# Performance work log

Hardware: AMD Instinct MI355X
Metric: run time of the kernel (lower is better)

Reference implementation:

```python
import jax, jax.numpy as jnp
import numpy as np

EP = 1e-4
MAX_ITER = 100
L = [512, 512]          # context lengths
C = 256                 # padded feature dim == total_dim
HEADS = 2


def nonsat_activation(x, ep=EP, max_iter=MAX_ITER):
    # Fixed-point iteration y <- (2y^3/3 + x)/(y^2+1), y0 = x.
    # Matches torch version: iterate on detached values, final update uses live x.
    xd = jax.lax.stop_gradient(x)
    f = lambda y: (2.0 * y ** 3 / 3.0 + xd) / (y ** 2 + 1.0)

    def cond(s):
        y, y_new, i = s
        return jnp.logical_and(jnp.mean(jnp.abs(y_new - y)) > ep, i <= max_iter)

    def body(s):
        y, y_new, i = s
        return (y_new, f(y_new), i + 1)

    y_prev, _, _ = jax.lax.while_loop(cond, body, (xd, f(xd), 0))
    y_prev = jax.lax.stop_gradient(y_prev)
    # final (returned) update, differentiable w.r.t. x only
    return (2.0 * y_prev ** 3 / 3.0 + x) / (y_prev ** 2 + 1.0)


def setup_inputs() -> dict:
    key = jax.random.key(0)
    k1, k2, k3 = jax.random.split(key, 3)
    x1 = jax.random.normal(k1, (32, 512, 256), dtype=jnp.float32)
    x2 = jax.random.normal(k2, (32, 512, 192), dtype=jnp.float32)
    # xavier_normal_ for U: std = sqrt(2/(fan_in+fan_out)) = sqrt(2/512) = 1/16
    U = jax.random.normal(k3, (HEADS, C, C), dtype=jnp.float32) * (1.0 / 16.0)
    return {"x1": x1, "x2": x2, "U": U}


def reference(x1, x2, U):
    # pad contexts to common feature dim C (zeros on the right)
    contexts = [x1, jnp.pad(x2, ((0, 0), (0, 0), (0, C - x2.shape[-1])))]
    q = sum(L)
    scaling = C ** (-0.5)
    M = jnp.concatenate(contexts, axis=1)  # (B, q, C)

    # mask uses sizes = L[1:] with blocks starting at offset 0 (faithful quirk)
    mask_mul = jnp.ones((q, q), dtype=jnp.float32).at[:L[1], :L[1]].set(0.0)

    h_reps = []
    mask_add = None
    for h in range(HEADS):
        # K[b,i,j] = sum_{c,d} M[b,i,c] U[h,c,d] M[b,j,d]
        K = jnp.einsum('bic,cd,bjd->bij', M, U[h], M) * scaling
        K = nonsat_activation(K)
        if mask_add is None:  # cached after head 0, reused for later heads
            mask_add = jnp.zeros((q, q), dtype=jnp.float32).at[:L[1], :L[1]].set(jnp.min(K))
        K_hat = K * mask_mul + mask_add
        cols = jnp.max(K_hat, axis=1)   # (B, q) max over rows per column
        rows = jnp.max(K_hat, axis=2)   # (B, q) max over cols per row
        alpha = rows + cols             # (B, q)
        reps = []
        offset = 0
        for i, Ci in enumerate(contexts):
            a = alpha[:, offset:offset + L[i]]          # (B, l_i)
            offset += L[i]
            wt = jax.nn.softmax(a, axis=1)              # (B, l_i)
            r = jnp.einsum('bl,blc->bc', wt, Ci)        # (B, C)
            reps.append(r)
        h_reps.append(jnp.stack(reps, axis=1))          # (B, N, C)
    return jnp.stack(h_reps, axis=0)                    # (heads, B, N, C)
```

## Files before the change

kernel.cpp:

```cpp
#include <hip/hip_runtime.h>
#include <math.h>

typedef _Float16 h16;
typedef h16  h16x8 __attribute__((ext_vector_type(8)));
typedef h16  h16x4 __attribute__((ext_vector_type(4)));
typedef float f32x4 __attribute__((ext_vector_type(4)));

#define MH_OFF   ((size_t)0)
#define ML_OFF   (MH_OFF + 16777216)
#define UHT_OFF  (ML_OFF + 16777216)
#define ULT_OFF  (UHT_OFF + 262144)
#define RMA_OFF  (ULT_OFF + 262144)
#define RMH_OFF  (RMA_OFF + 262144)
#define PCM_OFF  (RMH_OFF + 262144)
#define M0_OFF   (PCM_OFF + 4194304)

__device__ __forceinline__ float nonsat(float x) {
    float y = x;
#pragma unroll
    for (int i = 0; i < 24; ++i) {
        float y2 = y * y;
        y = fmaf(0.66666667f * y, y2, x) / (y2 + 1.0f);
    }
    return y;
}

__device__ __forceinline__ int fkey(float f) {
    const int i = __float_as_int(f);
    return (i >= 0) ? i : (i ^ 0x7fffffff);
}
__device__ __forceinline__ float funkey(int k) {
    return __int_as_float((k >= 0) ? k : (k ^ 0x7fffffff));
}

__global__ void k_prep(const float* __restrict__ x1, const float* __restrict__ x2,
                       const float* __restrict__ U, h16* __restrict__ MH,
                       h16* __restrict__ ML, h16* __restrict__ UHt,
                       h16* __restrict__ ULt, int* __restrict__ m0key,
                       float* __restrict__ out) {
    const int gid = blockIdx.x * 256 + threadIdx.x;
    if (blockIdx.x < 8192) {
        const int g  = gid;
        const int d4 = (g & 63) * 4;
        const int j  = (g >> 6) & 1023;
        const int b  = g >> 16;
        float v[4];
        if (j < 512) {
            const float4 p = *(const float4*)(x1 + ((size_t)(b * 512 + j) * 256 + d4));
            v[0] = p.x; v[1] = p.y; v[2] = p.z; v[3] = p.w;
        } else if (d4 < 192) {
            const float4 p = *(const float4*)(x2 +
                (size_t)(b * 512 + (j - 512)) * 192 + d4);
            v[0] = p.x; v[1] = p.y; v[2] = p.z; v[3] = p.w;
        } else {
            v[0] = v[1] = v[2] = v[3] = 0.0f;
        }
        h16x4 hh, ll;
#pragma unroll
        for (int k = 0; k < 4; ++k) {
            const h16 hi = (h16)v[k];
            hh[k] = hi;
            ll[k] = (h16)(v[k] - (float)hi);
        }
        const size_t o = (size_t)g * 4;
        *(h16x4*)&MH[o] = hh;
        *(h16x4*)&ML[o] = ll;
    } else if (blockIdx.x < 8320) {
        const int g  = gid - 8192 * 256;
        const int c4 = (g & 63) * 4;
        const int d  = (g >> 6) & 255;
        const int h  = g >> 14;
        h16x4 hh, ll;
#pragma unroll
        for (int k = 0; k < 4; ++k) {
            const float v = U[((size_t)h * 256 + c4 + k) * 256 + d] * 4.0f;
            const h16 hi = (h16)v;
            hh[k] = hi;
            ll[k] = (h16)(v - (float)hi);
        }
        const size_t o = ((size_t)h * 256 + d) * 256 + c4;
        *(h16x4*)&UHt[o] = hh;
        *(h16x4*)&ULt[o] = ll;
    } else {
        const int z = gid - 8320 * 256;
        out[z] = 0.0f;
        if (z == 0) *m0key = 0x7fffffff;
    }
}

__global__ __launch_bounds__(256, 2)
void k_main(const h16* __restrict__ MH, const h16* __restrict__ ML,
            const h16* __restrict__ UHt, const h16* __restrict__ ULt,
            float* __restrict__ rmax_all, float* __restrict__ rmax_hi,
            float* __restrict__ pcm, int* __restrict__ m0key) {
    __shared__ __align__(16) h16 sP[2][64 * 256];
    __shared__ float red[512 + 4];

    const int n    = blockIdx.x;
    const int x    = n & 7;
    const int s    = n >> 3;
    const int b    = x + 8 * (s >> 5);
    const int h    = (s >> 4) & 1;
    const int rblk = s & 15;
    const int hb   = h * 32 + b;
    const int r0   = rblk * 64;
    const int t    = threadIdx.x;
    const int w    = t >> 6;
    const int l    = t & 63;
    const int q    = l >> 4;
    const int ln   = l & 15;

    {
        f32x4 acc[4][4];
        const f32x4 z4 = {0.f, 0.f, 0.f, 0.f};
#pragma unroll
        for (int i = 0; i < 4; ++i)
#pragma unroll
            for (int j = 0; j < 4; ++j) acc[i][j] = z4;

        for (int kc = 0; kc < 8; ++kc) {
            const int c0 = kc * 32;
            h16x8 aH[4], aL[4], bH[4], bL[4];
#pragma unroll
            for (int ti = 0; ti < 4; ++ti) {
                const size_t off =
                    (size_t)(b * 1024 + r0 + ti * 16 + ln) * 256 + c0 + q * 8;
                aH[ti] = *(const h16x8*)&MH[off];
                aL[ti] = *(const h16x8*)&ML[off];
            }
#pragma unroll
            for (int tj = 0; tj < 4; ++tj) {
                const size_t off =
                    (size_t)(h * 256 + w * 64 + tj * 16 + ln) * 256 + c0 + q * 8;
                bH[tj] = *(const h16x8*)&UHt[off];
                bL[tj] = *(const h16x8*)&ULt[off];
            }
#pragma unroll
            for (int ti = 0; ti < 4; ++ti)
#pragma unroll
                for (int tj = 0; tj < 4; ++tj)
                    acc[ti][tj] = __builtin_amdgcn_mfma_f32_16x16x32_f16(
                        aH[ti], bH[tj], acc[ti][tj], 0, 0, 0);
#pragma unroll
            for (int ti = 0; ti < 4; ++ti)
#pragma unroll
                for (int tj = 0; tj < 4; ++tj)
                    acc[ti][tj] = __builtin_amdgcn_mfma_f32_16x16x32_f16(
                        aL[ti], bH[tj], acc[ti][tj], 0, 0, 0);
#pragma unroll
            for (int ti = 0; ti < 4; ++ti)
#pragma unroll
                for (int tj = 0; tj < 4; ++tj)
                    acc[ti][tj] = __builtin_amdgcn_mfma_f32_16x16x32_f16(
                        aH[ti], bL[tj], acc[ti][tj], 0, 0, 0);
        }
#pragma unroll
        for (int ti = 0; ti < 4; ++ti)
#pragma unroll
            for (int tj = 0; tj < 4; ++tj)
#pragma unroll
                for (int reg = 0; reg < 4; ++reg) {
                    const int r = ti * 16 + q * 4 + reg;
                    const int d = w * 64 + tj * 16 + ln;
                    const float v = acc[ti][tj][reg];
                    const h16 hi = (h16)v;
                    const h16 lo = (h16)(v - (float)hi);
                    const int off = r * 256 + (((d >> 3) ^ (r & 7)) << 3) + (d & 7);
                    sP[0][off] = hi;
                    sP[1][off] = lo;
                }
    }
    __syncthreads();

    float gmin = INFINITY;
    const int jts = (h == 1 && rblk < 8) ? 1 : 0;

    for (int jt = jts; jt < 2; ++jt) {
        const int jbase = jt * 512 + w * 128;
        const bool do_red = (rblk >= 8) || (jt == 1);
        f32x4 acc[4][8];
        const f32x4 z4 = {0.f, 0.f, 0.f, 0.f};
#pragma unroll
        for (int i = 0; i < 4; ++i)
#pragma unroll
            for (int j = 0; j < 8; ++j) acc[i][j] = z4;

        for (int kc = 0; kc < 8; ++kc) {
            const int d0 = kc * 32;
            h16x8 aH[4], aL[4], bb[8];
#pragma unroll
            for (int ti = 0; ti < 4; ++ti) {
                const int r = ti * 16 + ln;
                const int g = (kc * 4 + q) ^ (r & 7);
                aH[ti] = *(const h16x8*)&sP[0][r * 256 + g * 8];
                aL[ti] = *(const h16x8*)&sP[1][r * 256 + g * 8];
            }
#pragma unroll
            for (int tj = 0; tj < 8; ++tj)
                bb[tj] = *(const h16x8*)&MH[
                    (size_t)(b * 1024 + jbase + tj * 16 + ln) * 256 + d0 + q * 8];
#pragma unroll
            for (int tj = 0; tj < 8; ++tj)
#pragma unroll
                for (int ti = 0; ti < 4; ++ti)
                    acc[ti][tj] = __builtin_amdgcn_mfma_f32_16x16x32_f16(
                        aH[ti], bb[tj], acc[ti][tj], 0, 0, 0);
#pragma unroll
            for (int tj = 0; tj < 8; ++tj)
#pragma unroll
                for (int ti = 0; ti < 4; ++ti)
                    acc[ti][tj] = __builtin_amdgcn_mfma_f32_16x16x32_f16(
                        aL[ti], bb[tj], acc[ti][tj], 0, 0, 0);
#pragma unroll
            for (int tj = 0; tj < 8; ++tj)
                bb[tj] = *(const h16x8*)&ML[
                    (size_t)(b * 1024 + jbase + tj * 16 + ln) * 256 + d0 + q * 8];
#pragma unroll
            for (int tj = 0; tj < 8; ++tj)
#pragma unroll
                for (int ti = 0; ti < 4; ++ti)
                    acc[ti][tj] = __builtin_amdgcn_mfma_f32_16x16x32_f16(
                        aH[ti], bb[tj], acc[ti][tj], 0, 0, 0);
        }

        if (do_red) {
#pragma unroll
            for (int ti = 0; ti < 4; ++ti)
#pragma unroll
                for (int reg = 0; reg < 4; ++reg) {
                    float m = acc[ti][0][reg];
#pragma unroll
                    for (int tj = 1; tj < 8; ++tj) m = fmaxf(m, acc[ti][tj][reg]);
                    m = fmaxf(m, __shfl_xor(m, 1));
                    m = fmaxf(m, __shfl_xor(m, 2));
                    m = fmaxf(m, __shfl_xor(m, 4));
                    m = fmaxf(m, __shfl_xor(m, 8));
                    if (ln == 0)
                        red[(jt * 4 + w) * 64 + ti * 16 + q * 4 + reg] = m;
                }
#pragma unroll
            for (int tj = 0; tj < 8; ++tj) {
                float m = -INFINITY;
#pragma unroll
                for (int ti = 0; ti < 4; ++ti)
#pragma unroll
                    for (int reg = 0; reg < 4; ++reg) m = fmaxf(m, acc[ti][tj][reg]);
                m = fmaxf(m, __shfl_xor(m, 16));
                m = fmaxf(m, __shfl_xor(m, 32));
                if (q == 0)
                    pcm[(size_t)(hb * 16 + rblk) * 1024 + jbase + tj * 16 + ln] =
                        m * 0.015625f;
            }
        }
        if (h == 0) {
#pragma unroll
            for (int ti = 0; ti < 4; ++ti)
#pragma unroll
                for (int tj = 0; tj < 8; ++tj)
#pragma unroll
                    for (int reg = 0; reg < 4; ++reg)
                        gmin = fminf(gmin, acc[ti][tj][reg]);
        }
    }

#pragma unroll
    for (int off = 1; off < 64; off <<= 1) gmin = fminf(gmin, __shfl_xor(gmin, off));
    if (l == 0) red[512 + w] = gmin;
    __syncthreads();

    if (t < 64) {
        float hh = -INFINITY;
#pragma unroll
        for (int w2 = 0; w2 < 4; ++w2)
            hh = fmaxf(hh, red[(4 + w2) * 64 + t]);
        if (rblk < 8) {
            rmax_hi[(size_t)hb * 1024 + r0 + t] = hh * 0.015625f;
        } else {
            float a = hh;
#pragma unroll
            for (int w2 = 0; w2 < 4; ++w2)
                a = fmaxf(a, red[w2 * 64 + t]);
            rmax_all[(size_t)hb * 1024 + r0 + t] = a * 0.015625f;
        }
    }
    if (t == 0 && hb < 32) {
        const float g4 = fminf(fminf(red[512], red[513]),
                               fminf(red[514], red[515])) * 0.015625f;
        atomicMin(m0key, fkey(g4));
    }
}

__global__ __launch_bounds__(256)
void k_fin(const float* __restrict__ rmax_all, const float* __restrict__ rmax_hi,
           const float* __restrict__ pcm, const int* __restrict__ m0key,
           const float* __restrict__ x1, const float* __restrict__ x2,
           float* __restrict__ out) {
    __shared__ float wv[512];
    __shared__ float sm[4], ss[4];
    const int blk   = blockIdx.x;
    const int chunk = blk & 1;
    const int seg   = (blk >> 1) & 1;
    const int hb    = blk >> 2;
    const int b     = hb & 31;
    const int t     = threadIdx.x;
    const float m0  = funkey(*m0key);

    float a2[2];
#pragma unroll
    for (int half = 0; half < 2; ++half) {
        const int i = seg * 512 + half * 256 + t;
        float rraw;
        if (seg == 0) rraw = fmaxf(m0, rmax_hi[(size_t)hb * 1024 + i]);
        else          rraw = rmax_all[(size_t)hb * 1024 + i];
        float call = -INFINITY, chi = -INFINITY;
#pragma unroll
        for (int rb = 0; rb < 16; ++rb) {
            const float v = pcm[(size_t)(hb * 16 + rb) * 1024 + i];
            call = fmaxf(call, v);
            if (rb >= 8) chi = fmaxf(chi, v);
        }
        const float craw = (seg == 0) ? fmaxf(m0, chi) : call;
        a2[half] = nonsat(rraw) + nonsat(craw);
    }
    const float a0 = a2[0], a1 = a2[1];

    float m = fmaxf(a0, a1);
#pragma unroll
    for (int off = 1; off < 64; off <<= 1) m = fmaxf(m, __shfl_xor(m, off));
    if ((t & 63) == 0) sm[t >> 6] = m;
    __syncthreads();
    const float amax = fmaxf(fmaxf(sm[0], sm[1]), fmaxf(sm[2], sm[3]));

    const float e0 = __expf(a0 - amax), e1 = __expf(a1 - amax);
    wv[t] = e0; wv[t + 256] = e1;
    float s = e0 + e1;
#pragma unroll
    for (int off = 1; off < 64; off <<= 1) s += __shfl_xor(s, off);
    if ((t & 63) == 0) ss[t >> 6] = s;
    __syncthreads();
    const float inv = 1.0f / (ss[0] + ss[1] + ss[2] + ss[3]);

    const int lo = chunk * 256;
    float acc = 0.0f;
    if (seg == 0) {
        const float* xp = x1 + ((size_t)b * 512 + lo) * 256 + t;
#pragma unroll 4
        for (int l = 0; l < 256; ++l)
            acc = fmaf(wv[lo + l], xp[(size_t)l * 256], acc);
        atomicAdd(&out[(hb * 2 + seg) * 256 + t], acc * inv);
    } else if (t < 192) {
        const float* xp = x2 + ((size_t)b * 512 + lo) * 192 + t;
#pragma unroll 4
        for (int l = 0; l < 256; ++l)
            acc = fmaf(wv[lo + l], xp[(size_t)l * 192], acc);
        atomicAdd(&out[(hb * 2 + seg) * 256 + t], acc * inv);
    }
}

extern "C" void kernel_launch(void* const* d_in, const int* in_sizes, int n_in,
                              void* d_out, int out_size, void* d_ws, size_t ws_size,
                              hipStream_t stream) {
    const float* x1 = (const float*)d_in[0];
    const float* x2 = (const float*)d_in[1];
    const float* U  = (const float*)d_in[2];
    float* out = (float*)d_out;
    char* wsb  = (char*)d_ws;

    h16*   MHp  = (h16*)(wsb + MH_OFF);
    h16*   MLp  = (h16*)(wsb + ML_OFF);
    h16*   UHt  = (h16*)(wsb + UHT_OFF);
    h16*   ULt  = (h16*)(wsb + ULT_OFF);
    float* rma  = (float*)(wsb + RMA_OFF);
    float* rmh  = (float*)(wsb + RMH_OFF);
    float* pcm  = (float*)(wsb + PCM_OFF);
    int*   m0k  = (int*)(wsb + M0_OFF);

    hipLaunchKernelGGL(k_prep, dim3(8448), dim3(256), 0, stream, x1, x2, U,
                       MHp, MLp, UHt, ULt, m0k, out);
    hipLaunchKernelGGL(k_main, dim3(1024), dim3(256), 0, stream, MHp, MLp,
                       UHt, ULt, rma, rmh, pcm, m0k);
    hipLaunchKernelGGL(k_fin,  dim3(256),  dim3(256), 0, stream, rma, rmh,
                       pcm, m0k, x1, x2, out);
}
```

Before: 280.8 us.

## Split k_main work across 16 waves per block instead of 4

Raises the k_main block size from 256 to 1024 threads and redistributes both GEMM phases so each wave owns a smaller tile: the first phase splits 4 row tiles by 4 column groups, and the second gives each wave 32 columns instead of 128. Reduction buffers and final cross-wave reductions grow to cover 16 waves. The aim is to cut per-wave register pressure and give more latency hiding per CU. The cost is that each wave reloads the LDS A-fragments and now reuses them over only 2 B tiles, so operand reuse per MFMA drops. It also raises LDS read traffic and the barrier cost within a block.

```diff
diff --git a/kernel.cpp b/kernel.cpp
--- a/kernel.cpp
+++ b/kernel.cpp
@@ -88,13 +88,13 @@
     }
 }
 
-__global__ __launch_bounds__(256, 2)
+__global__ __launch_bounds__(1024, 4)
 void k_main(const h16* __restrict__ MH, const h16* __restrict__ ML,
             const h16* __restrict__ UHt, const h16* __restrict__ ULt,
             float* __restrict__ rmax_all, float* __restrict__ rmax_hi,
             float* __restrict__ pcm, int* __restrict__ m0key) {
     __shared__ __align__(16) h16 sP[2][64 * 256];
-    __shared__ float red[512 + 4];
+    __shared__ float red[2048 + 16];
 
     const int n    = blockIdx.x;
     const int x    = n & 7;
@@ -111,64 +111,54 @@
     const int ln   = l & 15;
 
     {
-        f32x4 acc[4][4];
+        const int wr = w >> 2, wc = w & 3;
+        f32x4 acc[4];
         const f32x4 z4 = {0.f, 0.f, 0.f, 0.f};
 #pragma unroll
-        for (int i = 0; i < 4; ++i)
-#pragma unroll
-            for (int j = 0; j < 4; ++j) acc[i][j] = z4;
+        for (int j = 0; j < 4; ++j) acc[j] = z4;
 
         for (int kc = 0; kc < 8; ++kc) {
             const int c0 = kc * 32;
-            h16x8 aH[4], aL[4], bH[4], bL[4];
-#pragma unroll
-            for (int ti = 0; ti < 4; ++ti) {
+            h16x8 aH, aL, bH[4], bL[4];
+            {
                 const size_t off =
-                    (size_t)(b * 1024 + r0 + ti * 16 + ln) * 256 + c0 + q * 8;
-                aH[ti] = *(const h16x8*)&MH[off];
-                aL[ti] = *(const h16x8*)&ML[off];
+                    (size_t)(b * 1024 + r0 + wr * 16 + ln) * 256 + c0 + q * 8;
+                aH = *(const h16x8*)&MH[off];
+                aL = *(const h16x8*)&ML[off];
             }
 #pragma unroll
             for (int tj = 0; tj < 4; ++tj) {
                 const size_t off =
-                    (size_t)(h * 256 + w * 64 + tj * 16 + ln) * 256 + c0 + q * 8;
+                    (size_t)(h * 256 + wc * 64 + tj * 16 + ln) * 256 + c0 + q * 8;
                 bH[tj] = *(const h16x8*)&UHt[off];
                 bL[tj] = *(const h16x8*)&ULt[off];
             }
 #pragma unroll
-            for (int ti = 0; ti < 4; ++ti)
-#pragma unroll
-                for (int tj = 0; tj < 4; ++tj)
-                    acc[ti][tj] = __builtin_amdgcn_mfma_f32_16x16x32_f16(
-                        aH[ti], bH[tj], acc[ti][tj], 0, 0, 0);
-#pragma unroll
-            for (int ti = 0; ti < 4; ++ti)
-#pragma unroll
-                for (int tj = 0; tj < 4; ++tj)
-                    acc[ti][tj] = __builtin_amdgcn_mfma_f32_16x16x32_f16(
-                        aL[ti], bH[tj], acc[ti][tj], 0, 0, 0);
-#pragma unroll
-            for (int ti = 0; ti < 4; ++ti)
-#pragma unroll
-                for (int tj = 0; tj < 4; ++tj)
-                    acc[ti][tj] = __builtin_amdgcn_mfma_f32_16x16x32_f16(
-                        aH[ti], bL[tj], acc[ti][tj], 0, 0, 0);
-        }
-#pragma unroll
-        for (int ti = 0; ti < 4; ++ti)
-#pragma unroll
             for (int tj = 0; tj < 4; ++tj)
-#pragma unroll
-                for (int reg = 0; reg < 4; ++reg) {
-                    const int r = ti * 16 + q * 4 + reg;
-                    const int d = w * 64 + tj * 16 + ln;
-                    const float v = acc[ti][tj][reg];
-                    const h16 hi = (h16)v;
-                    const h16 lo = (h16)(v - (float)hi);
-                    const int off = r * 256 + (((d >> 3) ^ (r & 7)) << 3) + (d & 7);
-                    sP[0][off] = hi;
-                    sP[1][off] = lo;
-                }
+                acc[tj] = __builtin_amdgcn_mfma_f32_16x16x32_f16(
+                    aH, bH[tj], acc[tj], 0, 0, 0);
+#pragma unroll
+            for (int tj = 0; tj < 4; ++tj)
+                acc[tj] = __builtin_amdgcn_mfma_f32_16x16x32_f16(
+                    aL, bH[tj], acc[tj], 0, 0, 0);
+#pragma unroll
+            for (int tj = 0; tj < 4; ++tj)
+                acc[tj] = __builtin_amdgcn_mfma_f32_16x16x32_f16(
+                    aH, bL[tj], acc[tj], 0, 0, 0);
+        }
+#pragma unroll
+        for (int tj = 0; tj < 4; ++tj)
+#pragma unroll
+            for (int reg = 0; reg < 4; ++reg) {
+                const int r = wr * 16 + q * 4 + reg;
+                const int d = wc * 64 + tj * 16 + ln;
+                const float v = acc[tj][reg];
+                const h16 hi = (h16)v;
+                const h16 lo = (h16)(v - (float)hi);
+                const int off = r * 256 + (((d >> 3) ^ (r & 7)) << 3) + (d & 7);
+                sP[0][off] = hi;
+                sP[1][off] = lo;
+            }
     }
     __syncthreads();
 
@@ -176,47 +166,47 @@
     const int jts = (h == 1 && rblk < 8) ? 1 : 0;
 
     for (int jt = jts; jt < 2; ++jt) {
-        const int jbase = jt * 512 + w * 128;
+        const int jbase = jt * 512 + w * 32;
         const bool do_red = (rblk >= 8) || (jt == 1);
-        f32x4 acc[4][8];
+        f32x4 acc[4][2];
         const f32x4 z4 = {0.f, 0.f, 0.f, 0.f};
 #pragma unroll
         for (int i = 0; i < 4; ++i)
 #pragma unroll
-            for (int j = 0; j < 8; ++j) acc[i][j] = z4;
+            for (int j = 0; j < 2; ++j) acc[i][j] = z4;
 
         for (int kc = 0; kc < 8; ++kc) {
             const int d0 = kc * 32;
-            h16x8 aH[4], aL[4], bb[8];
+            h16x8 aH[4], aL[4], bb[2];
+            const int g = ((kc * 4 + q) ^ (ln & 7)) * 8;
 #pragma unroll
             for (int ti = 0; ti < 4; ++ti) {
                 const int r = ti * 16 + ln;
-                const int g = (kc * 4 + q) ^ (r & 7);
-                aH[ti] = *(const h16x8*)&sP[0][r * 256 + g * 8];
-                aL[ti] = *(const h16x8*)&sP[1][r * 256 + g * 8];
-            }
-#pragma unroll
-            for (int tj = 0; tj < 8; ++tj)
+                aH[ti] = *(const h16x8*)&sP[0][r * 256 + g];
+                aL[ti] = *(const h16x8*)&sP[1][r * 256 + g];
+            }
+#pragma unroll
+            for (int tj = 0; tj < 2; ++tj)
                 bb[tj] = *(const h16x8*)&MH[
                     (size_t)(b * 1024 + jbase + tj * 16 + ln) * 256 + d0 + q * 8];
 #pragma unroll
-            for (int tj = 0; tj < 8; ++tj)
+            for (int tj = 0; tj < 2; ++tj)
 #pragma unroll
                 for (int ti = 0; ti < 4; ++ti)
                     acc[ti][tj] = __builtin_amdgcn_mfma_f32_16x16x32_f16(
                         aH[ti], bb[tj], acc[ti][tj], 0, 0, 0);
 #pragma unroll
-            for (int tj = 0; tj < 8; ++tj)
+            for (int tj = 0; tj < 2; ++tj)
 #pragma unroll
                 for (int ti = 0; ti < 4; ++ti)
                     acc[ti][tj] = __builtin_amdgcn_mfma_f32_16x16x32_f16(
                         aL[ti], bb[tj], acc[ti][tj], 0, 0, 0);
 #pragma unroll
-            for (int tj = 0; tj < 8; ++tj)
+            for (int tj = 0; tj < 2; ++tj)
                 bb[tj] = *(const h16x8*)&ML[
                     (size_t)(b * 1024 + jbase + tj * 16 + ln) * 256 + d0 + q * 8];
 #pragma unroll
-            for (int tj = 0; tj < 8; ++tj)
+            for (int tj = 0; tj < 2; ++tj)
 #pragma unroll
                 for (int ti = 0; ti < 4; ++ti)
                     acc[ti][tj] = __builtin_amdgcn_mfma_f32_16x16x32_f16(
@@ -228,18 +218,16 @@
             for (int ti = 0; ti < 4; ++ti)
 #pragma unroll
                 for (int reg = 0; reg < 4; ++reg) {
-                    float m = acc[ti][0][reg];
-#pragma unroll
-                    for (int tj = 1; tj < 8; ++tj) m = fmaxf(m, acc[ti][tj][reg]);
+                    float m = fmaxf(acc[ti][0][reg], acc[ti][1][reg]);
                     m = fmaxf(m, __shfl_xor(m, 1));
                     m = fmaxf(m, __shfl_xor(m, 2));
                     m = fmaxf(m, __shfl_xor(m, 4));
                     m = fmaxf(m, __shfl_xor(m, 8));
                     if (ln == 0)
-                        red[(jt * 4 + w) * 64 + ti * 16 + q * 4 + reg] = m;
+                        red[(jt * 16 + w) * 64 + ti * 16 + q * 4 + reg] = m;
                 }
 #pragma unroll
-            for (int tj = 0; tj < 8; ++tj) {
+            for (int tj = 0; tj < 2; ++tj) {
                 float m = -INFINITY;
 #pragma unroll
                 for (int ti = 0; ti < 4; ++ti)
@@ -256,7 +244,7 @@
 #pragma unroll
             for (int ti = 0; ti < 4; ++ti)
 #pragma unroll
-                for (int tj = 0; tj < 8; ++tj)
+                for (int tj = 0; tj < 2; ++tj)
 #pragma unroll
                     for (int reg = 0; reg < 4; ++reg)
                         gmin = fminf(gmin, acc[ti][tj][reg]);
@@ -265,28 +253,29 @@
 
 #pragma unroll
     for (int off = 1; off < 64; off <<= 1) gmin = fminf(gmin, __shfl_xor(gmin, off));
-    if (l == 0) red[512 + w] = gmin;
+    if (l == 0) red[2048 + w] = gmin;
     __syncthreads();
 
     if (t < 64) {
         float hh = -INFINITY;
 #pragma unroll
-        for (int w2 = 0; w2 < 4; ++w2)
-            hh = fmaxf(hh, red[(4 + w2) * 64 + t]);
+        for (int w2 = 0; w2 < 16; ++w2)
+            hh = fmaxf(hh, red[(16 + w2) * 64 + t]);
         if (rblk < 8) {
             rmax_hi[(size_t)hb * 1024 + r0 + t] = hh * 0.015625f;
         } else {
             float a = hh;
 #pragma unroll
-            for (int w2 = 0; w2 < 4; ++w2)
+            for (int w2 = 0; w2 < 16; ++w2)
                 a = fmaxf(a, red[w2 * 64 + t]);
             rmax_all[(size_t)hb * 1024 + r0 + t] = a * 0.015625f;
         }
     }
     if (t == 0 && hb < 32) {
-        const float g4 = fminf(fminf(red[512], red[513]),
-                               fminf(red[514], red[515])) * 0.015625f;
-        atomicMin(m0key, fkey(g4));
+        float g4 = red[2048];
+#pragma unroll
+        for (int i = 1; i < 16; ++i) g4 = fminf(g4, red[2048 + i]);
+        atomicMin(m0key, fkey(g4 * 0.015625f));
     }
 }
 
@@ -377,7 +366,7 @@
 
     hipLaunchKernelGGL(k_prep, dim3(8448), dim3(256), 0, stream, x1, x2, U,
                        MHp, MLp, UHt, ULt, m0k, out);
-    hipLaunchKernelGGL(k_main, dim3(1024), dim3(256), 0, stream, MHp, MLp,
+    hipLaunchKernelGGL(k_main, dim3(1024), dim3(1024), 0, stream, MHp, MLp,
                        UHt, ULt, rma, rmh, pcm, m0k);
     hipLaunchKernelGGL(k_fin,  dim3(256),  dim3(256), 0, stream, rma, rmh,
                        pcm, m0k, x1, x2, out);
```

Result: slower. 836.6 us (+198.0%).

## Double-buffer M tiles in LDS via async global_load_lds with 512-thread blocks

Applied to the files above, without the earlier changes.

The second GEMM stage no longer reads M hi/lo fragments straight from global memory per wave. Each k-step's 256x32 hi/lo tile is now staged into a double-buffered LDS area with global_load_lds, issued one step ahead. Blocks grow to 512 threads split as a 2x4 wave grid, so each wave holds a smaller accumulator tile. Row and column max reductions are restructured around this, with column maxima merged through shared memory. In exchange there is a barrier every k-step, much larger LDS use that may cap residency at one block per CU, possible bank conflicts on the 64-byte-stride tile reads, and reliance on barrier-implied waits for the async LDS loads.

```diff
diff --git a/kernel.cpp b/kernel.cpp
--- a/kernel.cpp
+++ b/kernel.cpp
@@ -88,13 +88,35 @@
     }
 }
 
-__global__ __launch_bounds__(256, 2)
+__device__ __forceinline__ void stage_b(const h16* __restrict__ MH,
+                                        const h16* __restrict__ ML,
+                                        h16* sBf, int buf, int b, int jt,
+                                        int jtile, int kc, int t, int w) {
+    const int jrow0 = jt * 512 + jtile * 256;
+#pragma unroll
+    for (int g = 0; g < 2; ++g) {
+        const size_t src = (size_t)(b * 1024 + jrow0 + g * 128 + (t >> 2)) * 256
+                           + kc * 32 + (t & 3) * 8;
+        h16* dH = sBf + (size_t)(buf * 2 + 0) * 8192 + g * 4096 + w * 512;
+        h16* dL = sBf + (size_t)(buf * 2 + 1) * 8192 + g * 4096 + w * 512;
+        __builtin_amdgcn_global_load_lds(
+            (const __attribute__((address_space(1))) void*)(MH + src),
+            (__attribute__((address_space(3))) void*)dH, 16, 0, 0);
+        __builtin_amdgcn_global_load_lds(
+            (const __attribute__((address_space(1))) void*)(ML + src),
+            (__attribute__((address_space(3))) void*)dL, 16, 0, 0);
+    }
+}
+
+__global__ __launch_bounds__(512, 2)
 void k_main(const h16* __restrict__ MH, const h16* __restrict__ ML,
             const h16* __restrict__ UHt, const h16* __restrict__ ULt,
             float* __restrict__ rmax_all, float* __restrict__ rmax_hi,
             float* __restrict__ pcm, int* __restrict__ m0key) {
     __shared__ __align__(16) h16 sP[2][64 * 256];
-    __shared__ float red[512 + 4];
+    __shared__ __align__(16) h16 sB[2 * 2 * 8192];
+    __shared__ float red[1024 + 8];
+    __shared__ float scm[2][512];
 
     const int n    = blockIdx.x;
     const int x    = n & 7;
@@ -109,60 +131,68 @@
     const int l    = t & 63;
     const int q    = l >> 4;
     const int ln   = l & 15;
+    const int wr   = w >> 2;
+    const int wj   = w & 3;
+
+    const int jts    = (h == 1 && rblk < 8) ? 1 : 0;
+    const int Usteps = (2 - jts) * 16;
+
+    stage_b(MH, ML, sB, 0, b, jts, 0, 0, t, w);
 
     {
-        f32x4 acc[4][4];
+        const int wrA = w >> 2, wcA = w & 3;
+        f32x4 accA[2][4];
         const f32x4 z4 = {0.f, 0.f, 0.f, 0.f};
 #pragma unroll
-        for (int i = 0; i < 4; ++i)
-#pragma unroll
-            for (int j = 0; j < 4; ++j) acc[i][j] = z4;
+        for (int i = 0; i < 2; ++i)
+#pragma unroll
+            for (int j2 = 0; j2 < 4; ++j2) accA[i][j2] = z4;
 
         for (int kc = 0; kc < 8; ++kc) {
             const int c0 = kc * 32;
-            h16x8 aH[4], aL[4], bH[4], bL[4];
-#pragma unroll
-            for (int ti = 0; ti < 4; ++ti) {
+            h16x8 aH[2], aL[2], bH[4], bL[4];
+#pragma unroll
+            for (int ti = 0; ti < 2; ++ti) {
                 const size_t off =
-                    (size_t)(b * 1024 + r0 + ti * 16 + ln) * 256 + c0 + q * 8;
+                    (size_t)(b * 1024 + r0 + wrA * 32 + ti * 16 + ln) * 256 + c0 + q * 8;
                 aH[ti] = *(const h16x8*)&MH[off];
                 aL[ti] = *(const h16x8*)&ML[off];
             }
 #pragma unroll
             for (int tj = 0; tj < 4; ++tj) {
                 const size_t off =
-                    (size_t)(h * 256 + w * 64 + tj * 16 + ln) * 256 + c0 + q * 8;
+                    (size_t)(h * 256 + wcA * 64 + tj * 16 + ln) * 256 + c0 + q * 8;
                 bH[tj] = *(const h16x8*)&UHt[off];
                 bL[tj] = *(const h16x8*)&ULt[off];
             }
 #pragma unroll
-            for (int ti = 0; ti < 4; ++ti)
+            for (int ti = 0; ti < 2; ++ti)
 #pragma unroll
                 for (int tj = 0; tj < 4; ++tj)
-                    acc[ti][tj] = __builtin_amdgcn_mfma_f32_16x16x32_f16(
-                        aH[ti], bH[tj], acc[ti][tj], 0, 0, 0);
-#pragma unroll
-            for (int ti = 0; ti < 4; ++ti)
+                    accA[ti][tj] = __builtin_amdgcn_mfma_f32_16x16x32_f16(
+                        aH[ti], bH[tj], accA[ti][tj], 0, 0, 0);
+#pragma unroll
+            for (int ti = 0; ti < 2; ++ti)
 #pragma unroll
                 for (int tj = 0; tj < 4; ++tj)
-                    acc[ti][tj] = __builtin_amdgcn_mfma_f32_16x16x32_f16(
-                        aL[ti], bH[tj], acc[ti][tj], 0, 0, 0);
-#pragma unroll
-            for (int ti = 0; ti < 4; ++ti)
+                    accA[ti][tj] = __builtin_amdgcn_mfma_f32_16x16x32_f16(
+                        aL[ti], bH[tj], accA[ti][tj], 0, 0, 0);
+#pragma unroll
+            for (int ti = 0; ti < 2; ++ti)
 #pragma unroll
                 for (int tj = 0; tj < 4; ++tj)
-                    acc[ti][tj] = __builtin_amdgcn_mfma_f32_16x16x32_f16(
-                        aH[ti], bL[tj], acc[ti][tj], 0, 0, 0);
-        }
-#pragma unroll
-        for (int ti = 0; ti < 4; ++ti)
+                    accA[ti][tj] = __builtin_amdgcn_mfma_f32_16x16x32_f16(
+                        aH[ti], bL[tj], accA[ti][tj], 0, 0, 0);
+        }
+#pragma unroll
+        for (int ti = 0; ti < 2; ++ti)
 #pragma unroll
             for (int tj = 0; tj < 4; ++tj)
 #pragma unroll
                 for (int reg = 0; reg < 4; ++reg) {
-                    const int r = ti * 16 + q * 4 + reg;
-                    const int d = w * 64 + tj * 16 + ln;
-                    const float v = acc[ti][tj][reg];
+                    const int r = wrA * 32 + ti * 16 + q * 4 + reg;
+                    const int d = wcA * 64 + tj * 16 + ln;
+                    const float v = accA[ti][tj][reg];
                     const h16 hi = (h16)v;
                     const h16 lo = (h16)(v - (float)hi);
                     const int off = r * 256 + (((d >> 3) ^ (r & 7)) << 3) + (d & 7);
@@ -173,120 +203,151 @@
     __syncthreads();
 
     float gmin = INFINITY;
-    const int jts = (h == 1 && rblk < 8) ? 1 : 0;
-
-    for (int jt = jts; jt < 2; ++jt) {
-        const int jbase = jt * 512 + w * 128;
-        const bool do_red = (rblk >= 8) || (jt == 1);
-        f32x4 acc[4][8];
-        const f32x4 z4 = {0.f, 0.f, 0.f, 0.f};
-#pragma unroll
-        for (int i = 0; i < 4; ++i)
-#pragma unroll
-            for (int j = 0; j < 8; ++j) acc[i][j] = z4;
-
-        for (int kc = 0; kc < 8; ++kc) {
-            const int d0 = kc * 32;
-            h16x8 aH[4], aL[4], bb[8];
-#pragma unroll
-            for (int ti = 0; ti < 4; ++ti) {
-                const int r = ti * 16 + ln;
-                const int g = (kc * 4 + q) ^ (r & 7);
-                aH[ti] = *(const h16x8*)&sP[0][r * 256 + g * 8];
-                aL[ti] = *(const h16x8*)&sP[1][r * 256 + g * 8];
+    float rm[2][4];
+    f32x4 acc[2][4];
+    const f32x4 z4 = {0.f, 0.f, 0.f, 0.f};
+    int cur = 0;
+
+#pragma unroll 1
+    for (int u = 0; u < Usteps; ++u) {
+        const int jt    = jts + (u >> 4);
+        const int jtile = (u >> 3) & 1;
+        const int kc    = u & 7;
+        const bool dored = (rblk >= 8) || (jt == 1);
+
+        if (u + 1 < Usteps) {
+            const int u1 = u + 1;
+            stage_b(MH, ML, sB, cur ^ 1, b, jts + (u1 >> 4), (u1 >> 3) & 1,
+                    u1 & 7, t, w);
+        }
+        if (kc == 0) {
+#pragma unroll
+            for (int i = 0; i < 2; ++i)
+#pragma unroll
+                for (int j2 = 0; j2 < 4; ++j2) acc[i][j2] = z4;
+            if (jtile == 0) {
+#pragma unroll
+                for (int i = 0; i < 2; ++i)
+#pragma unroll
+                    for (int j2 = 0; j2 < 4; ++j2) rm[i][j2] = -INFINITY;
             }
-#pragma unroll
-            for (int tj = 0; tj < 8; ++tj)
-                bb[tj] = *(const h16x8*)&MH[
-                    (size_t)(b * 1024 + jbase + tj * 16 + ln) * 256 + d0 + q * 8];
-#pragma unroll
-            for (int tj = 0; tj < 8; ++tj)
-#pragma unroll
-                for (int ti = 0; ti < 4; ++ti)
-                    acc[ti][tj] = __builtin_amdgcn_mfma_f32_16x16x32_f16(
-                        aH[ti], bb[tj], acc[ti][tj], 0, 0, 0);
-#pragma unroll
-            for (int tj = 0; tj < 8; ++tj)
-#pragma unroll
-                for (int ti = 0; ti < 4; ++ti)
-                    acc[ti][tj] = __builtin_amdgcn_mfma_f32_16x16x32_f16(
-                        aL[ti], bb[tj], acc[ti][tj], 0, 0, 0);
-#pragma unroll
-            for (int tj = 0; tj < 8; ++tj)
-                bb[tj] = *(const h16x8*)&ML[
-                    (size_t)(b * 1024 + jbase + tj * 16 + ln) * 256 + d0 + q * 8];
-#pragma unroll
-            for (int tj = 0; tj < 8; ++tj)
-#pragma unroll
-                for (int ti = 0; ti < 4; ++ti)
-                    acc[ti][tj] = __builtin_amdgcn_mfma_f32_16x16x32_f16(
-                        aH[ti], bb[tj], acc[ti][tj], 0, 0, 0);
-        }
-
-        if (do_red) {
-#pragma unroll
-            for (int ti = 0; ti < 4; ++ti)
-#pragma unroll
-                for (int reg = 0; reg < 4; ++reg) {
-                    float m = acc[ti][0][reg];
-#pragma unroll
-                    for (int tj = 1; tj < 8; ++tj) m = fmaxf(m, acc[ti][tj][reg]);
-                    m = fmaxf(m, __shfl_xor(m, 1));
-                    m = fmaxf(m, __shfl_xor(m, 2));
-                    m = fmaxf(m, __shfl_xor(m, 4));
-                    m = fmaxf(m, __shfl_xor(m, 8));
-                    if (ln == 0)
-                        red[(jt * 4 + w) * 64 + ti * 16 + q * 4 + reg] = m;
+        }
+
+        h16x8 aH[2], aL[2], bH[4], bL[4];
+#pragma unroll
+        for (int ti = 0; ti < 2; ++ti) {
+            const int r = wr * 32 + ti * 16 + ln;
+            const int g = ((kc * 4 + q) ^ (r & 7)) * 8;
+            aH[ti] = *(const h16x8*)&sP[0][r * 256 + g];
+            aL[ti] = *(const h16x8*)&sP[1][r * 256 + g];
+        }
+#pragma unroll
+        for (int tj = 0; tj < 4; ++tj) {
+            const int jr = wj * 64 + tj * 16 + ln;
+            bH[tj] = *(const h16x8*)&sB[(size_t)(cur * 2 + 0) * 8192 + jr * 32 + q * 8];
+            bL[tj] = *(const h16x8*)&sB[(size_t)(cur * 2 + 1) * 8192 + jr * 32 + q * 8];
+        }
+#pragma unroll
+        for (int tj = 0; tj < 4; ++tj)
+#pragma unroll
+            for (int ti = 0; ti < 2; ++ti)
+                acc[ti][tj] = __builtin_amdgcn_mfma_f32_16x16x32_f16(
+                    aH[ti], bH[tj], acc[ti][tj], 0, 0, 0);
+#pragma unroll
+        for (int tj = 0; tj < 4; ++tj)
+#pragma unroll
+            for (int ti = 0; ti < 2; ++ti)
+                acc[ti][tj] = __builtin_amdgcn_mfma_f32_16x16x32_f16(
+                    aL[ti], bH[tj], acc[ti][tj], 0, 0, 0);
+#pragma unroll
+        for (int tj = 0; tj < 4; ++tj)
+#pragma unroll
+            for (int ti = 0; ti < 2; ++ti)
+                acc[ti][tj] = __builtin_amdgcn_mfma_f32_16x16x32_f16(
+                    aH[ti], bL[tj], acc[ti][tj], 0, 0, 0);
+
+        if (kc == 7) {
+            if (dored) {
+#pragma unroll
+                for (int ti = 0; ti < 2; ++ti)
+#pragma unroll
+                    for (int reg = 0; reg < 4; ++reg) {
+                        float m = acc[ti][0][reg];
+#pragma unroll
+                        for (int tj = 1; tj < 4; ++tj) m = fmaxf(m, acc[ti][tj][reg]);
+                        m = fmaxf(m, __shfl_xor(m, 1));
+                        m = fmaxf(m, __shfl_xor(m, 2));
+                        m = fmaxf(m, __shfl_xor(m, 4));
+                        m = fmaxf(m, __shfl_xor(m, 8));
+                        rm[ti][reg] = fmaxf(rm[ti][reg], m);
+                    }
+                if (jtile == 1) {
+#pragma unroll
+                    for (int ti = 0; ti < 2; ++ti)
+#pragma unroll
+                        for (int reg = 0; reg < 4; ++reg)
+                            if (ln == 0)
+                                red[(jt * 8 + w) * 64 + wr * 32 + ti * 16 +
+                                    q * 4 + reg] = rm[ti][reg];
                 }
 #pragma unroll
-            for (int tj = 0; tj < 8; ++tj) {
-                float m = -INFINITY;
-#pragma unroll
-                for (int ti = 0; ti < 4; ++ti)
-#pragma unroll
-                    for (int reg = 0; reg < 4; ++reg) m = fmaxf(m, acc[ti][tj][reg]);
-                m = fmaxf(m, __shfl_xor(m, 16));
-                m = fmaxf(m, __shfl_xor(m, 32));
-                if (q == 0)
-                    pcm[(size_t)(hb * 16 + rblk) * 1024 + jbase + tj * 16 + ln] =
-                        m * 0.015625f;
+                for (int tj = 0; tj < 4; ++tj) {
+                    float m = -INFINITY;
+#pragma unroll
+                    for (int ti = 0; ti < 2; ++ti)
+#pragma unroll
+                        for (int reg = 0; reg < 4; ++reg)
+                            m = fmaxf(m, acc[ti][tj][reg]);
+                    m = fmaxf(m, __shfl_xor(m, 16));
+                    m = fmaxf(m, __shfl_xor(m, 32));
+                    if (q == 0)
+                        scm[wr][jtile * 256 + wj * 64 + tj * 16 + ln] = m;
+                }
             }
-        }
-        if (h == 0) {
-#pragma unroll
-            for (int ti = 0; ti < 4; ++ti)
-#pragma unroll
-                for (int tj = 0; tj < 8; ++tj)
-#pragma unroll
-                    for (int reg = 0; reg < 4; ++reg)
-                        gmin = fminf(gmin, acc[ti][tj][reg]);
+            if (h == 0) {
+#pragma unroll
+                for (int ti = 0; ti < 2; ++ti)
+#pragma unroll
+                    for (int tj = 0; tj < 4; ++tj)
+#pragma unroll
+                        for (int reg = 0; reg < 4; ++reg)
+                            gmin = fminf(gmin, acc[ti][tj][reg]);
+            }
+        }
+        __syncthreads();
+        cur ^= 1;
+        if ((u & 15) == 15 && dored) {
+            const float v = fmaxf(scm[0][t], scm[1][t]);
+            pcm[(size_t)(hb * 16 + rblk) * 1024 + jt * 512 + t] = v * 0.015625f;
         }
     }
 
 #pragma unroll
     for (int off = 1; off < 64; off <<= 1) gmin = fminf(gmin, __shfl_xor(gmin, off));
-    if (l == 0) red[512 + w] = gmin;
+    if (l == 0) red[1024 + w] = gmin;
     __syncthreads();
 
     if (t < 64) {
+        const int wrr = t >> 5;
         float hh = -INFINITY;
 #pragma unroll
         for (int w2 = 0; w2 < 4; ++w2)
-            hh = fmaxf(hh, red[(4 + w2) * 64 + t]);
+            hh = fmaxf(hh, red[(8 + wrr * 4 + w2) * 64 + t]);
         if (rblk < 8) {
             rmax_hi[(size_t)hb * 1024 + r0 + t] = hh * 0.015625f;
         } else {
             float a = hh;
 #pragma unroll
             for (int w2 = 0; w2 < 4; ++w2)
-                a = fmaxf(a, red[w2 * 64 + t]);
+                a = fmaxf(a, red[(wrr * 4 + w2) * 64 + t]);
             rmax_all[(size_t)hb * 1024 + r0 + t] = a * 0.015625f;
         }
     }
     if (t == 0 && hb < 32) {
-        const float g4 = fminf(fminf(red[512], red[513]),
-                               fminf(red[514], red[515])) * 0.015625f;
-        atomicMin(m0key, fkey(g4));
+        float g4 = red[1024];
+#pragma unroll
+        for (int i = 1; i < 8; ++i) g4 = fminf(g4, red[1024 + i]);
+        atomicMin(m0key, fkey(g4 * 0.015625f));
     }
 }
 
@@ -377,7 +438,7 @@
 
     hipLaunchKernelGGL(k_prep, dim3(8448), dim3(256), 0, stream, x1, x2, U,
                        MHp, MLp, UHt, ULt, m0k, out);
-    hipLaunchKernelGGL(k_main, dim3(1024), dim3(256), 0, stream, MHp, MLp,
+    hipLaunchKernelGGL(k_main, dim3(1024), dim3(512), 0, stream, MHp, MLp,
                        UHt, ULt, rma, rmh, pcm, m0k);
     hipLaunchKernelGGL(k_fin,  dim3(256),  dim3(256), 0, stream, rma, rmh,
                        pcm, m0k, x1, x2, out);
```

New measurement: 318.1 us. 1.13x slower.
